# Optimization experiments

Measured on AMD Instinct MI355X. Metric: run time of the kernel, lower is better.

## Reference

```python
import jax, jax.numpy as jnp
import numpy as np


def setup_inputs() -> dict:
    key = jax.random.key(0)
    kq, kk, kv = jax.random.split(key, 3)
    B, S, D = 4, 4096, 128
    return {
        "q_proj": jax.random.normal(kq, (B, S, D), dtype=jnp.float32),
        "k_proj": jax.random.normal(kk, (B, S, D), dtype=jnp.float32),
        "v_proj": jax.random.normal(kv, (B, S, D), dtype=jnp.float32),
    }


def reference(q_proj, k_proj, v_proj):
    # Block-wise online softmax in the original is mathematically exact
    # full (non-causal) scaled dot-product attention.
    d = q_proj.shape[-1]
    scale = 1.0 / jnp.sqrt(jnp.asarray(d, dtype=q_proj.dtype))
    logits = jnp.einsum('bqd,bkd->bqk', q_proj, k_proj) * scale  # [B,S,S]
    attn = jax.nn.softmax(logits, axis=-1)
    return jnp.einsum('bqk,bkd->bqd', attn, v_proj)
```

## Files before the change

### kernel.cpp

```cpp
#include <hip/hip_runtime.h>
#include <hip/hip_bf16.h>
#include <stdint.h>

#define Bn 4
#define Sn 4096
#define Dn 128
#define SCALE ((float)(0.08838834764831843 * 1.4426950408889634))

typedef __attribute__((ext_vector_type(8)))  short short8;
typedef __attribute__((ext_vector_type(4)))  short short4v;
typedef __attribute__((ext_vector_type(4)))  float f32x4;
typedef __attribute__((ext_vector_type(16))) float f32x16;
typedef __attribute__((ext_vector_type(2)))  uint32_t uint2v;

__device__ __forceinline__ uint32_t bfround(float f){
  union { float f; uint32_t u; } a; a.f = f;
  return a.u + 0x7FFFu + ((a.u >> 16) & 1u);
}
__device__ __forceinline__ uint32_t f2bf2(float lo, float hi){
  return (bfround(hi) & 0xFFFF0000u) | (bfround(lo) >> 16);
}
__device__ __forceinline__ uint32_t f2bf2_fast(float lo, float hi){
  const uint32_t a = __float_as_uint(lo) + 0x8000u;
  const uint32_t b = __float_as_uint(hi) + 0x8000u;
  return __builtin_amdgcn_perm(b, a, 0x07060302u);
}
__device__ __forceinline__ float bf2f(short s){
  union { uint32_t u; float f; } a; a.u = ((uint32_t)(unsigned short)s) << 16; return a.f;
}
__device__ __forceinline__ float fexp2(float x){
#if __has_builtin(__builtin_amdgcn_exp2f)
  return __builtin_amdgcn_exp2f(x);
#else
  return exp2f(x);
#endif
}

__device__ __forceinline__ void gload16(const void* g, void* l){
  __builtin_amdgcn_global_load_lds(
      (const __attribute__((address_space(1))) unsigned int*)g,
      (__attribute__((address_space(3))) unsigned int*)l, 16, 0, 0);
}

__global__ void prep_kernel(const float* __restrict__ k, const float* __restrict__ v,
                            short* __restrict__ kb, short* __restrict__ vt){
  const int bid = blockIdx.x;
  const int t   = threadIdx.x;
  if (bid < 2048){
    const int i = bid*256 + t;
    const f32x4 val = ((const f32x4*)k)[i];
    uint2v o;
    o[0] = f2bf2(val[0], val[1]);
    o[1] = f2bf2(val[2], val[3]);
    *(uint2v*)(kb + 4*(size_t)i) = o;
  } else {
    __shared__ float tile[64][65];
    const int vb = bid - 2048;
    const int s0 = (vb & 63) * 64;
    const int d0 = ((vb >> 6) & 1) * 64;
    const int b  = vb >> 7;
#pragma unroll
    for (int i=0;i<16;++i){
      int lin = i*256 + t;
      int r = lin >> 6, c = lin & 63;
      tile[r][c] = v[((size_t)(b*Sn + s0 + r))*Dn + d0 + c];
    }
    __syncthreads();
#pragma unroll
    for (int i=0;i<2;++i){
      int lin = i*256 + t;
      int r = lin >> 3;
      int u = lin & 7;
      union { uint32_t w[4]; short8 s; } pk;
#pragma unroll
      for (int p=0;p<4;++p){
        int x0 = u*8 + 2*p, x1 = x0 + 1;
        int k0 = (x0 & ~15) | ((x0 & 3) | (((x0>>2)&1)<<3) | (((x0>>3)&1)<<2));
        int k1 = (x1 & ~15) | ((x1 & 3) | (((x1>>2)&1)<<3) | (((x1>>3)&1)<<2));
        pk.w[p] = f2bf2(tile[k0][r], tile[k1][r]);
      }
      *(short8*)(vt + ((size_t)(b*Dn + d0 + r))*Sn + s0 + u*8) = pk.s;
    }
  }
}

__global__ __launch_bounds__(128, 1) void fa_kernel(
    const float* __restrict__ Qg, const short* __restrict__ Kb,
    const short* __restrict__ VTb, short* __restrict__ parts,
    float* __restrict__ lparts){
  __shared__ __align__(16) char lds[32768];
  const int tid = threadIdx.x;
  const int w = tid >> 6, lane = tid & 63;
  const int ln = lane & 31, h5 = lane >> 5;
  const int idx = blockIdx.x;
  const int b   = idx & 3;
  const int u2  = idx >> 2;
  const int qt  = u2 & 31;
  const int ks  = u2 >> 5;
  const int q0  = qt * 128;
  const int start_it = ks * 32;
  const int n_it     = 32;

  short8 Qf[2][8];
#pragma unroll
  for (int tile=0;tile<2;++tile){
    const float* qp = Qg + ((size_t)(b*Sn + q0 + w*64 + tile*32 + ln))*Dn;
#pragma unroll
    for (int t=0;t<8;++t){
      const int d0 = t*16 + h5*8;
      const f32x4 a = *(const f32x4*)(qp + d0);
      const f32x4 c = *(const f32x4*)(qp + d0 + 4);
      union { uint32_t u[4]; short8 s; } pk;
      pk.u[0] = f2bf2(a[0]*SCALE, a[1]*SCALE);
      pk.u[1] = f2bf2(a[2]*SCALE, a[3]*SCALE);
      pk.u[2] = f2bf2(c[0]*SCALE, c[1]*SCALE);
      pk.u[3] = f2bf2(c[2]*SCALE, c[3]*SCALE);
      Qf[tile][t] = pk.s;
    }
  }

  f32x16 Ot[2][4];
#pragma unroll
  for (int tile=0;tile<2;++tile)
#pragma unroll
    for (int m=0;m<4;++m)
#pragma unroll
      for (int r=0;r<16;++r) Ot[tile][m][r] = 0.0f;
  float lsA0=0.f, lsB0=0.f, lsA1=0.f, lsB1=0.f;

  int goffb, loffb;
  const char* gbase;
  if (w == 0){
    const int l4 = lane >> 4;
    goffb = l4*256 + (((lane & 15) ^ l4) * 16);
    loffb = lane*16;
    gbase = (const char*)Kb + ((size_t)(b*Sn + start_it*32))*256;
  } else {
    goffb = (lane >> 2)*8192 + ((((lane & 3) ^ ((lane >> 3) & 3))) * 16);
    loffb = 8192 + lane*16;
    gbase = (const char*)VTb + (size_t)b*Dn*Sn*2 + (size_t)start_it*64;
  }

  auto stage = [&](int i, int ph){
    char* ldsb = lds + ph*16384 + loffb;
    if (w == 0){
      const char* gb = gbase + (size_t)i*8192;
#pragma unroll
      for (int u=0;u<8;++u)
        gload16(gb + u*1024 + (goffb ^ ((u & 1) << 6)), ldsb + u*1024);
    } else {
      const char* gb = gbase + (size_t)i*64;
#pragma unroll
      for (int u=0;u<8;++u)
        gload16(gb + u*131072 + goffb, ldsb + u*1024);
    }
  };

  stage(0, 0);

  for (int i=0; i<n_it; ++i){
    const int ph = i & 1;
    __syncthreads();
    if (i+1 < n_it) stage(i+1, ph^1);

    const char* bK = lds + ph*16384;
    const char* bV = bK + 8192;

    f32x16 St0, St1;
#pragma unroll
    for (int r=0;r<16;++r){ St0[r] = 0.0f; St1[r] = 0.0f; }
    __builtin_amdgcn_s_setprio(1);
#pragma unroll
    for (int t=0;t<8;++t){
      const int pos = ((2*t + h5) ^ (ln & 7)) * 16;
      const short8 kf = *(const short8*)(bK + (size_t)ln*256 + pos);
      St0 = __builtin_amdgcn_mfma_f32_32x32x16_bf16(kf, Qf[0][t], St0, 0, 0, 0);
      St1 = __builtin_amdgcn_mfma_f32_32x32x16_bf16(kf, Qf[1][t], St1, 0, 0, 0);
    }
    __builtin_amdgcn_s_setprio(0);

#pragma unroll
    for (int r=0;r<16;++r) St0[r] = fexp2(St0[r]);
#pragma unroll
    for (int r=0;r<16;++r) St1[r] = fexp2(St1[r]);
#pragma unroll
    for (int r=0;r<16;r+=2){
      lsA0 += St0[r]; lsB0 += St0[r+1];
      lsA1 += St1[r]; lsB1 += St1[r+1];
    }

    union { uint32_t u[4]; short8 s; } pf0[2], pf1[2];
#pragma unroll
    for (int t=0;t<2;++t){
      pf0[t].u[0] = f2bf2_fast(St0[8*t+0], St0[8*t+1]);
      pf0[t].u[1] = f2bf2_fast(St0[8*t+2], St0[8*t+3]);
      pf0[t].u[2] = f2bf2_fast(St0[8*t+4], St0[8*t+5]);
      pf0[t].u[3] = f2bf2_fast(St0[8*t+6], St0[8*t+7]);
      pf1[t].u[0] = f2bf2_fast(St1[8*t+0], St1[8*t+1]);
      pf1[t].u[1] = f2bf2_fast(St1[8*t+2], St1[8*t+3]);
      pf1[t].u[2] = f2bf2_fast(St1[8*t+4], St1[8*t+5]);
      pf1[t].u[3] = f2bf2_fast(St1[8*t+6], St1[8*t+7]);
    }

    __builtin_amdgcn_s_setprio(1);
#pragma unroll
    for (int t=0;t<2;++t){
      const int phys = ((2*t + h5) ^ ((ln >> 1) & 3)) * 16;
#pragma unroll
      for (int mt=0;mt<4;++mt){
        const short8 vf = *(const short8*)(bV + (size_t)(mt*32+ln)*64 + phys);
        Ot[0][mt] = __builtin_amdgcn_mfma_f32_32x32x16_bf16(vf, pf0[t].s, Ot[0][mt], 0, 0, 0);
        Ot[1][mt] = __builtin_amdgcn_mfma_f32_32x32x16_bf16(vf, pf1[t].s, Ot[1][mt], 0, 0, 0);
      }
    }
    __builtin_amdgcn_s_setprio(0);
  }

  float lsum0 = lsA0 + lsB0; lsum0 += __shfl_xor(lsum0, 32, 64);
  float lsum1 = lsA1 + lsB1; lsum1 += __shfl_xor(lsum1, 32, 64);

  const int pslot = (b*32 + qt)*4 + ks;
#pragma unroll
  for (int tile=0;tile<2;++tile){
    short* pbase = parts + (size_t)pslot*16384 + (size_t)(w*64 + tile*32 + ln)*128;
#pragma unroll
    for (int mt=0;mt<4;++mt){
#pragma unroll
      for (int g=0;g<4;++g){
        union { uint32_t u[2]; short4v s; } o;
        o.u[0] = f2bf2(Ot[tile][mt][4*g],   Ot[tile][mt][4*g+1]);
        o.u[1] = f2bf2(Ot[tile][mt][4*g+2], Ot[tile][mt][4*g+3]);
        *(short4v*)(pbase + mt*32 + 8*g + 4*h5) = o.s;
      }
    }
  }
  if (h5 == 0){
    lparts[(size_t)pslot*128 + w*64 + ln]      = lsum0;
    lparts[(size_t)pslot*128 + w*64 + 32 + ln] = lsum1;
  }
}

__global__ void reduce_kernel(const short* __restrict__ parts,
                              const float* __restrict__ lparts,
                              float* __restrict__ out){
  const int t  = threadIdx.x;
  const int s  = blockIdx.x >> 3;
  const int qg = (blockIdx.x & 7)*16 + (t >> 4);
  const int d0 = (t & 15) * 8;
  float acc[8];
#pragma unroll
  for (int j=0;j<8;++j) acc[j] = 0.0f;
  float lsum = 0.0f;
#pragma unroll
  for (int ks=0;ks<4;++ks){
    const short8 p = *(const short8*)(parts + ((size_t)(s*4+ks))*16384 + (size_t)qg*128 + d0);
#pragma unroll
    for (int j=0;j<8;++j) acc[j] += bf2f(p[j]);
    lsum += lparts[(size_t)(s*4+ks)*128 + qg];
  }
  const float linv = 1.0f / lsum;
  f32x4 o0, o1;
#pragma unroll
  for (int j=0;j<4;++j){ o0[j] = acc[j]*linv; o1[j] = acc[4+j]*linv; }
  float* op = out + ((size_t)(s*128 + qg))*128 + d0;
  *(f32x4*)op = o0;
  *(f32x4*)(op + 4) = o1;
}

extern "C" void kernel_launch(void* const* d_in, const int* in_sizes, int n_in,
                              void* d_out, int out_size, void* d_ws, size_t ws_size,
                              hipStream_t stream){
  const float* q = (const float*)d_in[0];
  const float* k = (const float*)d_in[1];
  const float* v = (const float*)d_in[2];
  float* out = (float*)d_out;
  char* ws = (char*)d_ws;
  short* kb     = (short*)ws;
  short* vt     = kb + (size_t)Bn*Sn*Dn;
  short* parts  = (short*)(ws + 8388608);
  float* lparts = (float*)(ws + 8388608 + 16777216);

  prep_kernel<<<2560, 256, 0, stream>>>(k, v, kb, vt);
  fa_kernel<<<512, 128, 0, stream>>>(q, kb, vt, parts, lparts);
  reduce_kernel<<<1024, 256, 0, stream>>>(parts, lparts, out);
}
```

Measured before the change: 130.8 us.

## Split fa_kernel work across four waves by partitioning the output head dimension

Doubles the block to 256 threads. Waves are paired on the same query rows, and each pair covers half of the output D columns in the PV product. K/V staging is also split across all four waves, so each wave issues half as many loads. QK^T and the softmax numerator are now computed twice, once by each wave pair, which trades extra S-matrix MFMA work for lower accumulator register pressure and more waves per CU. Launch bounds change from (128,1) to (256,2).

```diff
diff --git a/kernel.cpp b/kernel.cpp
--- a/kernel.cpp
+++ b/kernel.cpp
@@ -84,7 +84,7 @@
   }
 }
 
-__global__ __launch_bounds__(128, 1) void fa_kernel(
+__global__ __launch_bounds__(256, 2) void fa_kernel(
     const float* __restrict__ Qg, const short* __restrict__ Kb,
     const short* __restrict__ VTb, short* __restrict__ parts,
     float* __restrict__ lparts){
@@ -92,6 +92,7 @@
   const int tid = threadIdx.x;
   const int w = tid >> 6, lane = tid & 63;
   const int ln = lane & 31, h5 = lane >> 5;
+  const int wq = w & 1, wd = w >> 1;
   const int idx = blockIdx.x;
   const int b   = idx & 3;
   const int u2  = idx >> 2;
@@ -104,7 +105,7 @@
   short8 Qf[2][8];
 #pragma unroll
   for (int tile=0;tile<2;++tile){
-    const float* qp = Qg + ((size_t)(b*Sn + q0 + w*64 + tile*32 + ln))*Dn;
+    const float* qp = Qg + ((size_t)(b*Sn + q0 + wq*64 + tile*32 + ln))*Dn;
 #pragma unroll
     for (int t=0;t<8;++t){
       const int d0 = t*16 + h5*8;
@@ -119,41 +120,46 @@
     }
   }
 
-  f32x16 Ot[2][4];
+  f32x16 Ot[2][2];
 #pragma unroll
   for (int tile=0;tile<2;++tile)
 #pragma unroll
-    for (int m=0;m<4;++m)
+    for (int m=0;m<2;++m)
 #pragma unroll
       for (int r=0;r<16;++r) Ot[tile][m][r] = 0.0f;
   float lsA0=0.f, lsB0=0.f, lsA1=0.f, lsB1=0.f;
 
-  int goffb, loffb;
+  int soff[4], doff[4];
   const char* gbase;
-  if (w == 0){
+  size_t gstride;
+  if (w < 2){
     const int l4 = lane >> 4;
-    goffb = l4*256 + (((lane & 15) ^ l4) * 16);
-    loffb = lane*16;
+    const int goffb = l4*256 + (((lane & 15) ^ l4) * 16);
+#pragma unroll
+    for (int u=0;u<4;++u){
+      const int cu = w*4 + u;
+      soff[u] = cu*1024 + (goffb ^ ((cu & 1) << 6));
+      doff[u] = cu*1024 + lane*16;
+    }
     gbase = (const char*)Kb + ((size_t)(b*Sn + start_it*32))*256;
+    gstride = 8192;
   } else {
-    goffb = (lane >> 2)*8192 + ((((lane & 3) ^ ((lane >> 3) & 3))) * 16);
-    loffb = 8192 + lane*16;
+    const int goffb = (lane >> 2)*8192 + ((((lane & 3) ^ ((lane >> 3) & 3))) * 16);
+#pragma unroll
+    for (int u=0;u<4;++u){
+      const int cu = (w-2)*4 + u;
+      soff[u] = cu*131072 + goffb;
+      doff[u] = 8192 + cu*1024 + lane*16;
+    }
     gbase = (const char*)VTb + (size_t)b*Dn*Sn*2 + (size_t)start_it*64;
+    gstride = 64;
   }
 
   auto stage = [&](int i, int ph){
-    char* ldsb = lds + ph*16384 + loffb;
-    if (w == 0){
-      const char* gb = gbase + (size_t)i*8192;
-#pragma unroll
-      for (int u=0;u<8;++u)
-        gload16(gb + u*1024 + (goffb ^ ((u & 1) << 6)), ldsb + u*1024);
-    } else {
-      const char* gb = gbase + (size_t)i*64;
-#pragma unroll
-      for (int u=0;u<8;++u)
-        gload16(gb + u*131072 + goffb, ldsb + u*1024);
-    }
+    char* ldsb = lds + ph*16384;
+    const char* gb = gbase + (size_t)i*gstride;
+#pragma unroll
+    for (int u=0;u<4;++u) gload16(gb + soff[u], ldsb + doff[u]);
   };
 
   stage(0, 0);
@@ -207,10 +213,11 @@
     for (int t=0;t<2;++t){
       const int phys = ((2*t + h5) ^ ((ln >> 1) & 3)) * 16;
 #pragma unroll
-      for (int mt=0;mt<4;++mt){
+      for (int mtp=0;mtp<2;++mtp){
+        const int mt = wd*2 + mtp;
         const short8 vf = *(const short8*)(bV + (size_t)(mt*32+ln)*64 + phys);
-        Ot[0][mt] = __builtin_amdgcn_mfma_f32_32x32x16_bf16(vf, pf0[t].s, Ot[0][mt], 0, 0, 0);
-        Ot[1][mt] = __builtin_amdgcn_mfma_f32_32x32x16_bf16(vf, pf1[t].s, Ot[1][mt], 0, 0, 0);
+        Ot[0][mtp] = __builtin_amdgcn_mfma_f32_32x32x16_bf16(vf, pf0[t].s, Ot[0][mtp], 0, 0, 0);
+        Ot[1][mtp] = __builtin_amdgcn_mfma_f32_32x32x16_bf16(vf, pf1[t].s, Ot[1][mtp], 0, 0, 0);
       }
     }
     __builtin_amdgcn_s_setprio(0);
@@ -222,21 +229,22 @@
   const int pslot = (b*32 + qt)*4 + ks;
 #pragma unroll
   for (int tile=0;tile<2;++tile){
-    short* pbase = parts + (size_t)pslot*16384 + (size_t)(w*64 + tile*32 + ln)*128;
-#pragma unroll
-    for (int mt=0;mt<4;++mt){
+    short* pbase = parts + (size_t)pslot*16384 + (size_t)(wq*64 + tile*32 + ln)*128;
+#pragma unroll
+    for (int mtp=0;mtp<2;++mtp){
+      const int mt = wd*2 + mtp;
 #pragma unroll
       for (int g=0;g<4;++g){
         union { uint32_t u[2]; short4v s; } o;
-        o.u[0] = f2bf2(Ot[tile][mt][4*g],   Ot[tile][mt][4*g+1]);
-        o.u[1] = f2bf2(Ot[tile][mt][4*g+2], Ot[tile][mt][4*g+3]);
+        o.u[0] = f2bf2(Ot[tile][mtp][4*g],   Ot[tile][mtp][4*g+1]);
+        o.u[1] = f2bf2(Ot[tile][mtp][4*g+2], Ot[tile][mtp][4*g+3]);
         *(short4v*)(pbase + mt*32 + 8*g + 4*h5) = o.s;
       }
     }
   }
-  if (h5 == 0){
-    lparts[(size_t)pslot*128 + w*64 + ln]      = lsum0;
-    lparts[(size_t)pslot*128 + w*64 + 32 + ln] = lsum1;
+  if (wd == 0 && h5 == 0){
+    lparts[(size_t)pslot*128 + wq*64 + ln]      = lsum0;
+    lparts[(size_t)pslot*128 + wq*64 + 32 + ln] = lsum1;
   }
 }
 
@@ -281,6 +289,6 @@
   float* lparts = (float*)(ws + 8388608 + 16777216);
 
   prep_kernel<<<2560, 256, 0, stream>>>(k, v, kb, vt);
-  fa_kernel<<<512, 128, 0, stream>>>(q, kb, vt, parts, lparts);
+  fa_kernel<<<512, 256, 0, stream>>>(q, kb, vt, parts, lparts);
   reduce_kernel<<<1024, 256, 0, stream>>>(parts, lparts, out);
 }
```

Result: slower. 135.8 us (+3.8%).
